# Optimization experiments

Measured on AMD Instinct MI355X. Metric: run time of the kernel, lower is better.

The kernel has to match this reference:

```python
import jax, jax.numpy as jnp
import numpy as np

DIM = 1024
HEADS = 16
HIDDEN = 4 * DIM

def _gelu_erf(x):
    # GELU via erf, matching the torch module exactly
    return x * 0.5 * (1.0 + jax.lax.erf(x / jnp.sqrt(2.0).astype(x.dtype)))

def setup_inputs() -> dict:
    key = jax.random.key(0)
    ks = jax.random.split(key, 12)
    s = 0.02
    x = jax.random.normal(ks[0], (2, 2048, DIM), dtype=jnp.float32)
    # MHSA params
    ln1_g = jnp.ones((DIM,), jnp.float32)
    ln1_b = jnp.zeros((DIM,), jnp.float32)
    w_qkv = jax.random.normal(ks[1], (DIM, 3 * DIM), jnp.float32) * s  # no bias
    w_proj = jax.random.normal(ks[2], (DIM, DIM), jnp.float32) * s
    b_proj = jnp.zeros((DIM,), jnp.float32)
    # ResMLP params
    ln2_g = jnp.ones((DIM,), jnp.float32)
    ln2_b = jnp.zeros((DIM,), jnp.float32)
    w1 = jax.random.normal(ks[3], (DIM, HIDDEN), jnp.float32) * s
    b1 = jnp.zeros((HIDDEN,), jnp.float32)
    w2 = jax.random.normal(ks[4], (HIDDEN, DIM), jnp.float32) * s
    b2 = jnp.zeros((DIM,), jnp.float32)
    return {"x": x, "ln1_g": ln1_g, "ln1_b": ln1_b, "w_qkv": w_qkv,
            "w_proj": w_proj, "b_proj": b_proj, "ln2_g": ln2_g, "ln2_b": ln2_b,
            "w1": w1, "b1": b1, "w2": w2, "b2": b2}

def _layernorm(x, g, b, eps=1e-5):
    mu = jnp.mean(x, axis=-1, keepdims=True)
    var = jnp.mean(jnp.square(x - mu), axis=-1, keepdims=True)
    return (x - mu) * jax.lax.rsqrt(var + eps) * g + b

def reference(x, ln1_g, ln1_b, w_qkv, w_proj, b_proj, ln2_g, ln2_b, w1, b1, w2, b2):
    B, N, C = x.shape
    H = HEADS
    hd = C // H
    scale = hd ** -0.5
    # --- MHSA (dropout is identity in eval) ---
    h = _layernorm(x, ln1_g, ln1_b)
    qkv = (h @ w_qkv).reshape(B, N, 3, H, hd)
    q = jnp.transpose(qkv[:, :, 0], (0, 2, 1, 3))  # [B,H,N,hd]
    k = jnp.transpose(qkv[:, :, 1], (0, 2, 1, 3))
    v = jnp.transpose(qkv[:, :, 2], (0, 2, 1, 3))
    attn = jax.nn.softmax(jnp.einsum('bhnd,bhmd->bhnm', q, k) * scale, axis=-1)
    out = jnp.einsum('bhnm,bhmd->bhnd', attn, v)
    out = jnp.transpose(out, (0, 2, 1, 3)).reshape(B, N, C)
    x = x + out @ w_proj + b_proj
    # --- ResMLP ---
    h = _layernorm(x, ln2_g, ln2_b)
    h = _gelu_erf(h @ w1 + b1)
    x = x + h @ w2 + b2
    return x
```

## Files before the change

kernel.cpp:

```cpp
#include <hip/hip_runtime.h>
#include <stdint.h>


#define DIMC 1024
#define HIDN 4096
#define SEQ  2048
#define TOK  4096

typedef __bf16 bf16x8 __attribute__((ext_vector_type(8)));
typedef float  f32x4  __attribute__((ext_vector_type(4)));
typedef unsigned short ushort8 __attribute__((ext_vector_type(8)));

__device__ inline unsigned short f2bf(float f) {
  union { float f; unsigned u; } v; v.f = f;
  unsigned u = v.u;
  return (unsigned short)((u + 0x7fffu + ((u >> 16) & 1u)) >> 16);
}

__device__ inline unsigned cvt_pk_bf16(float a, float b) {
  unsigned r;
  asm("v_cvt_pk_bf16_f32 %0, %1, %2" : "=v"(r) : "v"(a), "v"(b));
  return r;
}

__device__ inline f32x4 mfma_bf16(bf16x8 a, bf16x8 b, f32x4 c) {
  return __builtin_amdgcn_mfma_f32_16x16x32_bf16(a, b, c, 0, 0, 0);
}

typedef const __attribute__((address_space(1))) unsigned int* as1_u32p;
typedef __attribute__((address_space(3))) unsigned int* as3_u32p;
__device__ inline void gload_lds16(const unsigned short* g, unsigned short* l) {
  __builtin_amdgcn_global_load_lds((as1_u32p)(const void*)g, (as3_u32p)(void*)l,
                                   16, 0, 0);
}

__global__ __launch_bounds__(256)
void transpose_cast4(const float* __restrict__ wa, unsigned short* __restrict__ ta,
                     const float* __restrict__ wb, unsigned short* __restrict__ tb,
                     const float* __restrict__ wc, unsigned short* __restrict__ tc,
                     const float* __restrict__ wd, unsigned short* __restrict__ td) {
  __shared__ float tile[32][33];
  const int bid = blockIdx.x;
  const float* w; unsigned short* wt; int K, N, bx, by;
  if (bid < 3072)      { w = wa; wt = ta; K = 1024; N = 3072; bx = bid % 96;  by = bid / 96; }
  else if (bid < 4096) { int i = bid - 3072; w = wb; wt = tb; K = 1024; N = 1024; bx = i % 32;  by = i / 32; }
  else if (bid < 8192) { int i = bid - 4096; w = wc; wt = tc; K = 1024; N = 4096; bx = i % 128; by = i / 128; }
  else                 { int i = bid - 8192; w = wd; wt = td; K = 4096; N = 1024; bx = i % 32;  by = i / 32; }
  const int k0 = by * 32;
  const int n0 = bx * 32;
  const int tx = threadIdx.x & 31;
  const int ty = threadIdx.x >> 5;
#pragma unroll
  for (int i = 0; i < 4; i++)
    tile[ty + i * 8][tx] = w[(size_t)(k0 + ty + i * 8) * N + n0 + tx];
  __syncthreads();
#pragma unroll
  for (int i = 0; i < 4; i++)
    wt[(size_t)(n0 + ty + i * 8) * K + k0 + tx] = f2bf(tile[tx][ty + i * 8]);
}

__global__ __launch_bounds__(256)
void ln_kernel(const float* __restrict__ x, const float* __restrict__ g,
               const float* __restrict__ b, unsigned short* __restrict__ out) {
  const int row = blockIdx.x;
  const int tid = threadIdx.x;
  const float4* xr = (const float4*)&x[(size_t)row * DIMC];
  float4 v = xr[tid];
  float s  = v.x + v.y + v.z + v.w;
  float sq = v.x * v.x + v.y * v.y + v.z * v.z + v.w * v.w;
#pragma unroll
  for (int off = 32; off > 0; off >>= 1) {
    s  += __shfl_xor(s, off, 64);
    sq += __shfl_xor(sq, off, 64);
  }
  __shared__ float red[8];
  if ((tid & 63) == 0) { red[tid >> 6] = s; red[4 + (tid >> 6)] = sq; }
  __syncthreads();
  s  = red[0] + red[1] + red[2] + red[3];
  sq = red[4] + red[5] + red[6] + red[7];
  const float mu  = s * (1.0f / DIMC);
  const float var = sq * (1.0f / DIMC) - mu * mu;
  const float rs  = rsqrtf(var + 1e-5f);
  const int c = tid * 4;
  float vv[4] = {v.x, v.y, v.z, v.w};
#pragma unroll
  for (int j = 0; j < 4; j++)
    out[(size_t)row * DIMC + c + j] = f2bf((vv[j] - mu) * rs * g[c + j] + b[c + j]);
}

template <int EPI, int TN>
__global__ __launch_bounds__(256, (TN == 64) ? 4 : 2)
void gemm_bt(const unsigned short* __restrict__ A,
             const unsigned short* __restrict__ Bt,
             float* __restrict__ Cf, unsigned short* __restrict__ Cb,
             const float* __restrict__ bias, const float* __restrict__ res,
             int M, int N, int K) {
  constexpr int NU = TN / 32;
  constexpr int BP = TN / 32;
  __shared__ unsigned short As[128 * 64];
  __shared__ unsigned short Bs[TN * 64];
  const int gx  = N / TN;
  const int bid = blockIdx.x;
  const int xcd = bid & 7;
  const int lin = bid >> 3;
  const int bx  = lin % gx;
  const int by  = (xcd << 2) + lin / gx;
  const int tid  = threadIdx.x;
  const int lane = tid & 63;
  const int wave = tid >> 6;
  const int m0 = by * 128;
  const int n0 = bx * TN;
  const int wm = (wave >> 1) * 64;
  const int wn = (wave & 1) * (TN / 2);
  const int lm = lane & 15;
  const int lg = lane >> 4;
  const int r8 = tid >> 3;
  const int c8 = tid & 7;
  const int csrc = ((c8 ^ (r8 & 7)) * 8);

  const unsigned short* gA = &A [(size_t)(m0 + r8) * K + csrc];
  const unsigned short* gB = &Bt[(size_t)(n0 + r8) * K + csrc];

  f32x4 acc[4][NU];
#pragma unroll
  for (int t = 0; t < 4; t++)
#pragma unroll
    for (int u = 0; u < NU; u++) acc[t][u] = {0.f, 0.f, 0.f, 0.f};

  const int x0 = (lg ^ (lm & 7)) * 8;
  const int x1 = ((4 + lg) ^ (lm & 7)) * 8;

  for (int k0 = 0; k0 < K; k0 += 64) {
    __syncthreads();
#pragma unroll
    for (int p = 0; p < 4; p++)
      gload_lds16(gA + (size_t)p * 32 * K + k0, &As[p * 2048 + wave * 512]);
#pragma unroll
    for (int p = 0; p < BP; p++)
      gload_lds16(gB + (size_t)p * 32 * K + k0, &Bs[p * 2048 + wave * 512]);
    __syncthreads();
#pragma unroll
    for (int sub = 0; sub < 2; sub++) {
      const int xo = sub ? x1 : x0;
      bf16x8 af[4], bfr[NU];
#pragma unroll
      for (int t = 0; t < 4; t++)  af[t]  = *(const bf16x8*)&As[(wm + t * 16 + lm) * 64 + xo];
#pragma unroll
      for (int u = 0; u < NU; u++) bfr[u] = *(const bf16x8*)&Bs[(wn + u * 16 + lm) * 64 + xo];
#pragma unroll
      for (int t = 0; t < 4; t++)
#pragma unroll
        for (int u = 0; u < NU; u++)
          acc[t][u] = mfma_bf16(af[t], bfr[u], acc[t][u]);
    }
  }

#pragma unroll
  for (int t = 0; t < 4; t++) {
    const int row = m0 + wm + t * 16 + lg * 4;
#pragma unroll
    for (int u = 0; u < NU; u++) {
      const int col = n0 + wn + u * 16 + lm;
#pragma unroll
      for (int r = 0; r < 4; r++) {
        float v = acc[t][u][r];
        size_t idx = (size_t)(row + r) * N + col;
        if (EPI == 0) {
          const float sc = (col < 1024) ? 0.18033688011112042f : 1.0f;
          Cb[idx] = f2bf(v * sc);
        } else if (EPI == 1) {
          Cf[idx] = v + bias[col] + res[idx];
        } else {
          float xg = v + bias[col];
          Cb[idx] = f2bf(0.5f * xg * (1.0f + erff(xg * 0.70710678118654752f)));
        }
      }
    }
  }
}

__global__ __launch_bounds__(256)
void repack_kv(const unsigned short* __restrict__ qkv,
               unsigned short* __restrict__ kT, unsigned short* __restrict__ vT) {
  const int kt = blockIdx.x;
  const int bh = blockIdx.y;
  const int b = bh >> 4, h = bh & 15;
  const int tid = threadIdx.x;
  __shared__ unsigned short tile[64 * 72];
  const int tok = tid >> 2;
  const int ch  = tid & 3;
  const size_t srow = (size_t)(b * SEQ + kt * 64 + tok) * 3072 + h * 64;
  ushort8 ka = *(const ushort8*)&qkv[srow + 1024 + ch * 8];
  ushort8 kb = *(const ushort8*)&qkv[srow + 1024 + 32 + ch * 8];
  const size_t kdst = ((size_t)bh * SEQ + kt * 64 + tok) * 64;
  *(ushort8*)&kT[kdst + ch * 8] = ka;
  *(ushort8*)&kT[kdst + 32 + ch * 8] = kb;
  ushort8 va = *(const ushort8*)&qkv[srow + 2048 + ch * 8];
  ushort8 vb = *(const ushort8*)&qkv[srow + 2048 + 32 + ch * 8];
  *(ushort8*)&tile[tok * 72 + ch * 8] = va;
  *(ushort8*)&tile[tok * 72 + 32 + ch * 8] = vb;
  __syncthreads();
  const int d = tid >> 2;
  ushort8 o0, o1;
#pragma unroll
  for (int j = 0; j < 8; j++) {
    o0[j] = tile[(ch * 8 + j) * 72 + d];
    o1[j] = tile[((ch + 4) * 8 + j) * 72 + d];
  }
  const size_t vdst = ((size_t)bh * 64 + d) * SEQ + kt * 64;
  *(ushort8*)&vT[vdst + ch * 8] = o0;
  *(ushort8*)&vT[vdst + 32 + ch * 8] = o1;
}

__global__ __launch_bounds__(256)
void attn_kernel(const unsigned short* __restrict__ qkv,
                 const unsigned short* __restrict__ kT,
                 const unsigned short* __restrict__ vT,
                 unsigned short* __restrict__ out) {
  const int bid = blockIdx.x;
  const int xcd = bid & 7;
  const int lin = bid >> 3;
  const int bh  = (xcd << 2) + (lin >> 5);
  const int qt  = lin & 31;
  const int b  = bh >> 4;
  const int h  = bh & 15;
  const int tid  = threadIdx.x;
  const int lane = tid & 63;
  const int wave = tid >> 6;
  const int lm = lane & 15;
  const int lg = lane >> 4;

  __shared__ unsigned short Ks[64 * 64];
  __shared__ unsigned short Vs[64 * 64];
  __shared__ unsigned short Ps[4][16 * 64];

  const int qrow_base = b * SEQ + qt * 64 + wave * 16;
  bf16x8 qb[2];
#pragma unroll
  for (int c = 0; c < 2; c++)
    qb[c] = *(const bf16x8*)&qkv[(size_t)(qrow_base + lm) * 3072 + h * 64 + c * 32 + lg * 8];

  f32x4 o[4];
#pragma unroll
  for (int dt = 0; dt < 4; dt++) o[dt] = {0.f, 0.f, 0.f, 0.f};
  float li = 0.f;

  const unsigned short* kbp = &kT[(size_t)bh * SEQ * 64];
  const unsigned short* vbp = &vT[(size_t)bh * 64 * SEQ];
  const int srow = tid >> 3;
  const int slog = ((tid & 7) ^ (srow & 7)) * 8;
  const int xk0 = ((lg)     ^ (lm & 7)) * 8;
  const int xk1 = ((4 + lg) ^ (lm & 7)) * 8;

  for (int kt = 0; kt < SEQ / 64; kt++) {
    __syncthreads();
#pragma unroll
    for (int p = 0; p < 2; p++) {
      gload_lds16(&kbp[(size_t)kt * 4096 + (p * 32 + srow) * 64 + slog],
                  &Ks[p * 2048 + wave * 512]);
      gload_lds16(&vbp[(size_t)(p * 32 + srow) * SEQ + kt * 64 + slog],
                  &Vs[p * 2048 + wave * 512]);
    }
    __syncthreads();

    f32x4 st[4];
#pragma unroll
    for (int u = 0; u < 4; u++) {
      bf16x8 ka0 = *(const bf16x8*)&Ks[(u * 16 + lm) * 64 + xk0];
      bf16x8 ka1 = *(const bf16x8*)&Ks[(u * 16 + lm) * 64 + xk1];
      f32x4 z = {0.f, 0.f, 0.f, 0.f};
      z = mfma_bf16(ka0, qb[0], z);
      z = mfma_bf16(ka1, qb[1], z);
      st[u] = z;
    }

#pragma unroll
    for (int u = 0; u < 4; u++)
#pragma unroll
      for (int r = 0; r < 4; r++) {
        float p = exp2f(st[u][r] - 8.0f);
        st[u][r] = p;
        li += p;
      }

#pragma unroll
    for (int u = 0; u < 4; u++) {
      uint2 pk;
      pk.x = cvt_pk_bf16(st[u][0], st[u][1]);
      pk.y = cvt_pk_bf16(st[u][2], st[u][3]);
      const int phys = (u * 2 + (lg >> 1)) ^ (lm & 7);
      *(uint2*)&Ps[wave][lm * 64 + phys * 8 + (lg & 1) * 4] = pk;
    }

#pragma unroll
    for (int kc = 0; kc < 2; kc++) {
      const int xo = kc ? xk1 : xk0;
      bf16x8 pb = *(const bf16x8*)&Ps[wave][lm * 64 + xo];
#pragma unroll
      for (int dt = 0; dt < 4; dt++) {
        bf16x8 va = *(const bf16x8*)&Vs[(dt * 16 + lm) * 64 + xo];
        o[dt] = mfma_bf16(va, pb, o[dt]);
      }
    }
  }

  li += __shfl_xor(li, 16, 64);
  li += __shfl_xor(li, 32, 64);
  const float inv = 1.0f / li;
#pragma unroll
  for (int dt = 0; dt < 4; dt++) {
    uint2 ok;
    ok.x = cvt_pk_bf16(o[dt][0] * inv, o[dt][1] * inv);
    ok.y = cvt_pk_bf16(o[dt][2] * inv, o[dt][3] * inv);
    *(uint2*)&out[(size_t)(qrow_base + lm) * DIMC + h * 64 + dt * 16 + lg * 4] = ok;
  }
}

extern "C" void kernel_launch(void* const* d_in, const int* in_sizes, int n_in,
                              void* d_out, int out_size, void* d_ws, size_t ws_size,
                              hipStream_t stream) {
  const float* x      = (const float*)d_in[0];
  const float* ln1_g  = (const float*)d_in[1];
  const float* ln1_b  = (const float*)d_in[2];
  const float* w_qkv  = (const float*)d_in[3];
  const float* w_proj = (const float*)d_in[4];
  const float* b_proj = (const float*)d_in[5];
  const float* ln2_g  = (const float*)d_in[6];
  const float* ln2_b  = (const float*)d_in[7];
  const float* w1     = (const float*)d_in[8];
  const float* b1     = (const float*)d_in[9];
  const float* w2     = (const float*)d_in[10];
  const float* b2     = (const float*)d_in[11];
  float* out = (float*)d_out;

  char* ws = (char*)d_ws;
  size_t off = 0;
  auto alloc = [&](size_t bytes) { void* p = ws + off; off += (bytes + 255) & ~(size_t)255; return p; };
  unsigned short* wqkvT = (unsigned short*)alloc((size_t)3072 * 1024 * 2);
  unsigned short* wprjT = (unsigned short*)alloc((size_t)1024 * 1024 * 2);
  unsigned short* w1T   = (unsigned short*)alloc((size_t)4096 * 1024 * 2);
  unsigned short* w2T   = (unsigned short*)alloc((size_t)1024 * 4096 * 2);
  unsigned short* hb    = (unsigned short*)alloc((size_t)TOK * 1024 * 2);
  unsigned short* qkvb  = (unsigned short*)alloc((size_t)TOK * 3072 * 2);
  unsigned short* attnb = (unsigned short*)alloc((size_t)TOK * 1024 * 2);
  float*          x1    = (float*)         alloc((size_t)TOK * 1024 * 4);
  unsigned short* hidb  = (unsigned short*)alloc((size_t)TOK * 4096 * 2);
  unsigned short* kT = hidb;
  unsigned short* vT = hidb + (size_t)32 * SEQ * 64;

  transpose_cast4<<<12288, 256, 0, stream>>>(w_qkv, wqkvT, w_proj, wprjT,
                                             w1, w1T, w2, w2T);
  ln_kernel<<<TOK, 256, 0, stream>>>(x, ln1_g, ln1_b, hb);
  gemm_bt<0, 128><<<768, 256, 0, stream>>>(
      hb, wqkvT, nullptr, qkvb, nullptr, nullptr, TOK, 3072, 1024);
  repack_kv<<<dim3(SEQ / 64, 32), 256, 0, stream>>>(qkvb, kT, vT);
  attn_kernel<<<1024, 256, 0, stream>>>(qkvb, kT, vT, attnb);
  gemm_bt<1, 64><<<512, 256, 0, stream>>>(
      attnb, wprjT, x1, nullptr, b_proj, x, TOK, 1024, 1024);
  ln_kernel<<<TOK, 256, 0, stream>>>(x1, ln2_g, ln2_b, hb);
  gemm_bt<2, 128><<<1024, 256, 0, stream>>>(
      hb, w1T, nullptr, hidb, b1, nullptr, TOK, 4096, 1024);
  gemm_bt<1, 64><<<512, 256, 0, stream>>>(
      hidb, w2T, out, nullptr, b2, x1, TOK, 1024, 4096);
}
```

Baseline: 371.6 us.

## Fuse K/V repack into QKV GEMM epilogue and retile attention to 64 rows per wave

The QKV GEMM epilogue now scatters Q, K and transposed V straight into their attention layouts, which removes the separate repack kernel and the full qkv buffer round trip. The attention kernel moves to 128-thread blocks in which each wave handles 64 query rows, so every K/V tile loaded into LDS is reused four times. It also uses the hardware exp2 builtin and raises the occupancy hint for the TN=128 GEMMs. The trade-offs are scattered, uncoalesced 2-byte stores for transposed V, more register pressure in attention, and fewer attention blocks.

New measurement: 374.1 us. Within noise of the previous version (+0.7%).

```diff
diff --git a/kernel.cpp b/kernel.cpp
--- a/kernel.cpp
+++ b/kernel.cpp
@@ -22,6 +22,12 @@
   asm("v_cvt_pk_bf16_f32 %0, %1, %2" : "=v"(r) : "v"(a), "v"(b));
   return r;
 }
+
+#if __has_builtin(__builtin_amdgcn_exp2f)
+__device__ inline float fast_exp2(float x) { return __builtin_amdgcn_exp2f(x); }
+#else
+__device__ inline float fast_exp2(float x) { return exp2f(x); }
+#endif
 
 __device__ inline f32x4 mfma_bf16(bf16x8 a, bf16x8 b, f32x4 c) {
   return __builtin_amdgcn_mfma_f32_16x16x32_bf16(a, b, c, 0, 0, 0);
@@ -89,12 +95,15 @@
 }
 
 template <int EPI, int TN>
-__global__ __launch_bounds__(256, (TN == 64) ? 4 : 2)
+__global__ __launch_bounds__(256, (TN == 64) ? 4 : 3)
 void gemm_bt(const unsigned short* __restrict__ A,
              const unsigned short* __restrict__ Bt,
              float* __restrict__ Cf, unsigned short* __restrict__ Cb,
              const float* __restrict__ bias, const float* __restrict__ res,
-             int M, int N, int K) {
+             int M, int N, int K,
+             unsigned short* __restrict__ qd,
+             unsigned short* __restrict__ kTd,
+             unsigned short* __restrict__ vTd) {
   constexpr int NU = TN / 32;
   constexpr int BP = TN / 32;
   __shared__ unsigned short As[128 * 64];
@@ -166,8 +175,17 @@
         float v = acc[t][u][r];
         size_t idx = (size_t)(row + r) * N + col;
         if (EPI == 0) {
-          const float sc = (col < 1024) ? 0.18033688011112042f : 1.0f;
-          Cb[idx] = f2bf(v * sc);
+          const int rr = row + r;
+          const int bb = rr >> 11, key = rr & (SEQ - 1);
+          if (col < 1024) {
+            qd[(size_t)rr * 1024 + col] = f2bf(v * 0.18033688011112042f);
+          } else if (col < 2048) {
+            const int d = col - 1024, h = d >> 6, dd = d & 63;
+            kTd[(((size_t)(bb * 16 + h)) * SEQ + key) * 64 + dd] = f2bf(v);
+          } else {
+            const int d = col - 2048, h = d >> 6, dd = d & 63;
+            vTd[(((size_t)(bb * 16 + h)) * 64 + dd) * SEQ + key] = f2bf(v);
+          }
         } else if (EPI == 1) {
           Cf[idx] = v + bias[col] + res[idx];
         } else {
@@ -179,49 +197,16 @@
   }
 }
 
-__global__ __launch_bounds__(256)
-void repack_kv(const unsigned short* __restrict__ qkv,
-               unsigned short* __restrict__ kT, unsigned short* __restrict__ vT) {
-  const int kt = blockIdx.x;
-  const int bh = blockIdx.y;
-  const int b = bh >> 4, h = bh & 15;
-  const int tid = threadIdx.x;
-  __shared__ unsigned short tile[64 * 72];
-  const int tok = tid >> 2;
-  const int ch  = tid & 3;
-  const size_t srow = (size_t)(b * SEQ + kt * 64 + tok) * 3072 + h * 64;
-  ushort8 ka = *(const ushort8*)&qkv[srow + 1024 + ch * 8];
-  ushort8 kb = *(const ushort8*)&qkv[srow + 1024 + 32 + ch * 8];
-  const size_t kdst = ((size_t)bh * SEQ + kt * 64 + tok) * 64;
-  *(ushort8*)&kT[kdst + ch * 8] = ka;
-  *(ushort8*)&kT[kdst + 32 + ch * 8] = kb;
-  ushort8 va = *(const ushort8*)&qkv[srow + 2048 + ch * 8];
-  ushort8 vb = *(const ushort8*)&qkv[srow + 2048 + 32 + ch * 8];
-  *(ushort8*)&tile[tok * 72 + ch * 8] = va;
-  *(ushort8*)&tile[tok * 72 + 32 + ch * 8] = vb;
-  __syncthreads();
-  const int d = tid >> 2;
-  ushort8 o0, o1;
-#pragma unroll
-  for (int j = 0; j < 8; j++) {
-    o0[j] = tile[(ch * 8 + j) * 72 + d];
-    o1[j] = tile[((ch + 4) * 8 + j) * 72 + d];
-  }
-  const size_t vdst = ((size_t)bh * 64 + d) * SEQ + kt * 64;
-  *(ushort8*)&vT[vdst + ch * 8] = o0;
-  *(ushort8*)&vT[vdst + 32 + ch * 8] = o1;
-}
-
-__global__ __launch_bounds__(256)
-void attn_kernel(const unsigned short* __restrict__ qkv,
+__global__ __launch_bounds__(128, 2)
+void attn_kernel(const unsigned short* __restrict__ qbuf,
                  const unsigned short* __restrict__ kT,
                  const unsigned short* __restrict__ vT,
                  unsigned short* __restrict__ out) {
   const int bid = blockIdx.x;
   const int xcd = bid & 7;
   const int lin = bid >> 3;
-  const int bh  = (xcd << 2) + (lin >> 5);
-  const int qt  = lin & 31;
+  const int bh  = (xcd << 2) + (lin >> 4);
+  const int qt  = lin & 15;
   const int b  = bh >> 4;
   const int h  = bh & 15;
   const int tid  = threadIdx.x;
@@ -232,18 +217,23 @@
 
   __shared__ unsigned short Ks[64 * 64];
   __shared__ unsigned short Vs[64 * 64];
-  __shared__ unsigned short Ps[4][16 * 64];
-
-  const int qrow_base = b * SEQ + qt * 64 + wave * 16;
-  bf16x8 qb[2];
-#pragma unroll
-  for (int c = 0; c < 2; c++)
-    qb[c] = *(const bf16x8*)&qkv[(size_t)(qrow_base + lm) * 3072 + h * 64 + c * 32 + lg * 8];
-
-  f32x4 o[4];
-#pragma unroll
-  for (int dt = 0; dt < 4; dt++) o[dt] = {0.f, 0.f, 0.f, 0.f};
-  float li = 0.f;
+  __shared__ unsigned short Ps[2][64 * 64];
+
+  const int qrow_base = b * SEQ + qt * 128 + wave * 64;
+  bf16x8 qb[4][2];
+#pragma unroll
+  for (int s = 0; s < 4; s++)
+#pragma unroll
+    for (int c = 0; c < 2; c++)
+      qb[s][c] = *(const bf16x8*)&qbuf[(size_t)(qrow_base + s * 16 + lm) * 1024 +
+                                       h * 64 + c * 32 + lg * 8];
+
+  f32x4 o[4][4];
+#pragma unroll
+  for (int dt = 0; dt < 4; dt++)
+#pragma unroll
+    for (int s = 0; s < 4; s++) o[dt][s] = {0.f, 0.f, 0.f, 0.f};
+  float li[4] = {0.f, 0.f, 0.f, 0.f};
 
   const unsigned short* kbp = &kT[(size_t)bh * SEQ * 64];
   const unsigned short* vbp = &vT[(size_t)bh * 64 * SEQ];
@@ -255,64 +245,72 @@
   for (int kt = 0; kt < SEQ / 64; kt++) {
     __syncthreads();
 #pragma unroll
-    for (int p = 0; p < 2; p++) {
-      gload_lds16(&kbp[(size_t)kt * 4096 + (p * 32 + srow) * 64 + slog],
-                  &Ks[p * 2048 + wave * 512]);
-      gload_lds16(&vbp[(size_t)(p * 32 + srow) * SEQ + kt * 64 + slog],
-                  &Vs[p * 2048 + wave * 512]);
+    for (int p = 0; p < 4; p++) {
+      gload_lds16(&kbp[(size_t)kt * 4096 + (p * 16 + srow) * 64 + slog],
+                  &Ks[p * 1024 + wave * 512]);
+      gload_lds16(&vbp[(size_t)(p * 16 + srow) * SEQ + kt * 64 + slog],
+                  &Vs[p * 1024 + wave * 512]);
     }
     __syncthreads();
 
-    f32x4 st[4];
 #pragma unroll
     for (int u = 0; u < 4; u++) {
       bf16x8 ka0 = *(const bf16x8*)&Ks[(u * 16 + lm) * 64 + xk0];
       bf16x8 ka1 = *(const bf16x8*)&Ks[(u * 16 + lm) * 64 + xk1];
-      f32x4 z = {0.f, 0.f, 0.f, 0.f};
-      z = mfma_bf16(ka0, qb[0], z);
-      z = mfma_bf16(ka1, qb[1], z);
-      st[u] = z;
-    }
-
-#pragma unroll
-    for (int u = 0; u < 4; u++)
-#pragma unroll
-      for (int r = 0; r < 4; r++) {
-        float p = exp2f(st[u][r] - 8.0f);
-        st[u][r] = p;
-        li += p;
+      f32x4 st[4];
+#pragma unroll
+      for (int s = 0; s < 4; s++) {
+        f32x4 z = {0.f, 0.f, 0.f, 0.f};
+        z = mfma_bf16(ka0, qb[s][0], z);
+        z = mfma_bf16(ka1, qb[s][1], z);
+        st[s] = z;
       }
-
-#pragma unroll
-    for (int u = 0; u < 4; u++) {
-      uint2 pk;
-      pk.x = cvt_pk_bf16(st[u][0], st[u][1]);
-      pk.y = cvt_pk_bf16(st[u][2], st[u][3]);
-      const int phys = (u * 2 + (lg >> 1)) ^ (lm & 7);
-      *(uint2*)&Ps[wave][lm * 64 + phys * 8 + (lg & 1) * 4] = pk;
+#pragma unroll
+      for (int s = 0; s < 4; s++) {
+        float p0 = fast_exp2(st[s][0] - 8.0f);
+        float p1 = fast_exp2(st[s][1] - 8.0f);
+        float p2 = fast_exp2(st[s][2] - 8.0f);
+        float p3 = fast_exp2(st[s][3] - 8.0f);
+        li[s] += (p0 + p1) + (p2 + p3);
+        uint2 pk;
+        pk.x = cvt_pk_bf16(p0, p1);
+        pk.y = cvt_pk_bf16(p2, p3);
+        const int phys = (u * 2 + (lg >> 1)) ^ (lm & 7);
+        *(uint2*)&Ps[wave][(s * 16 + lm) * 64 + phys * 8 + (lg & 1) * 4] = pk;
+      }
     }
 
 #pragma unroll
     for (int kc = 0; kc < 2; kc++) {
       const int xo = kc ? xk1 : xk0;
-      bf16x8 pb = *(const bf16x8*)&Ps[wave][lm * 64 + xo];
+      bf16x8 pb[4];
+#pragma unroll
+      for (int s = 0; s < 4; s++)
+        pb[s] = *(const bf16x8*)&Ps[wave][(s * 16 + lm) * 64 + xo];
 #pragma unroll
       for (int dt = 0; dt < 4; dt++) {
         bf16x8 va = *(const bf16x8*)&Vs[(dt * 16 + lm) * 64 + xo];
-        o[dt] = mfma_bf16(va, pb, o[dt]);
+#pragma unroll
+        for (int s = 0; s < 4; s++)
+          o[dt][s] = mfma_bf16(va, pb[s], o[dt][s]);
       }
     }
   }
 
-  li += __shfl_xor(li, 16, 64);
-  li += __shfl_xor(li, 32, 64);
-  const float inv = 1.0f / li;
-#pragma unroll
-  for (int dt = 0; dt < 4; dt++) {
-    uint2 ok;
-    ok.x = cvt_pk_bf16(o[dt][0] * inv, o[dt][1] * inv);
-    ok.y = cvt_pk_bf16(o[dt][2] * inv, o[dt][3] * inv);
-    *(uint2*)&out[(size_t)(qrow_base + lm) * DIMC + h * 64 + dt * 16 + lg * 4] = ok;
+#pragma unroll
+  for (int s = 0; s < 4; s++) {
+    float l = li[s];
+    l += __shfl_xor(l, 16, 64);
+    l += __shfl_xor(l, 32, 64);
+    const float inv = 1.0f / l;
+#pragma unroll
+    for (int dt = 0; dt < 4; dt++) {
+      uint2 ok;
+      ok.x = cvt_pk_bf16(o[dt][s][0] * inv, o[dt][s][1] * inv);
+      ok.y = cvt_pk_bf16(o[dt][s][2] * inv, o[dt][s][3] * inv);
+      *(uint2*)&out[(size_t)(qrow_base + s * 16 + lm) * DIMC + h * 64 +
+                    dt * 16 + lg * 4] = ok;
+    }
   }
 }
 
@@ -341,7 +339,7 @@
   unsigned short* w1T   = (unsigned short*)alloc((size_t)4096 * 1024 * 2);
   unsigned short* w2T   = (unsigned short*)alloc((size_t)1024 * 4096 * 2);
   unsigned short* hb    = (unsigned short*)alloc((size_t)TOK * 1024 * 2);
-  unsigned short* qkvb  = (unsigned short*)alloc((size_t)TOK * 3072 * 2);
+  unsigned short* qbuf  = (unsigned short*)alloc((size_t)TOK * 1024 * 2);
   unsigned short* attnb = (unsigned short*)alloc((size_t)TOK * 1024 * 2);
   float*          x1    = (float*)         alloc((size_t)TOK * 1024 * 4);
   unsigned short* hidb  = (unsigned short*)alloc((size_t)TOK * 4096 * 2);
@@ -352,14 +350,17 @@
                                              w1, w1T, w2, w2T);
   ln_kernel<<<TOK, 256, 0, stream>>>(x, ln1_g, ln1_b, hb);
   gemm_bt<0, 128><<<768, 256, 0, stream>>>(
-      hb, wqkvT, nullptr, qkvb, nullptr, nullptr, TOK, 3072, 1024);
-  repack_kv<<<dim3(SEQ / 64, 32), 256, 0, stream>>>(qkvb, kT, vT);
-  attn_kernel<<<1024, 256, 0, stream>>>(qkvb, kT, vT, attnb);
+      hb, wqkvT, nullptr, nullptr, nullptr, nullptr, TOK, 3072, 1024,
+      qbuf, kT, vT);
+  attn_kernel<<<512, 128, 0, stream>>>(qbuf, kT, vT, attnb);
   gemm_bt<1, 64><<<512, 256, 0, stream>>>(
-      attnb, wprjT, x1, nullptr, b_proj, x, TOK, 1024, 1024);
+      attnb, wprjT, x1, nullptr, b_proj, x, TOK, 1024, 1024,
+      nullptr, nullptr, nullptr);
   ln_kernel<<<TOK, 256, 0, stream>>>(x1, ln2_g, ln2_b, hb);
   gemm_bt<2, 128><<<1024, 256, 0, stream>>>(
-      hb, w1T, nullptr, hidb, b1, nullptr, TOK, 4096, 1024);
+      hb, w1T, nullptr, hidb, b1, nullptr, TOK, 4096, 1024,
+      nullptr, nullptr, nullptr);
   gemm_bt<1, 64><<<512, 256, 0, stream>>>(
-      hidb, w2T, out, nullptr, b2, x1, TOK, 1024, 4096);
-}
+      hidb, w2T, out, nullptr, b2, x1, TOK, 1024, 4096,
+      nullptr, nullptr, nullptr);
+}
```
